# Performance work log

Hardware: AMD Instinct MI355X
Metric: run time of the kernel (lower is better)

## Reference

```python
import jax, jax.numpy as jnp
import numpy as np

NUM_USERS = 100000
NUM_ITEMS = 50000
DIM = 128
NUM_EDGES = 600000


def setup_inputs() -> dict:
    key = jax.random.key(0)
    k1, k2, k3, k4, k5, k6 = jax.random.split(key, 6)
    u_emb = jax.random.normal(k1, (NUM_USERS, DIM), dtype=jnp.float32)
    i_emb = jax.random.normal(k2, (NUM_ITEMS, DIM), dtype=jnp.float32)
    user_idx = jax.random.randint(k3, (NUM_EDGES,), 0, NUM_USERS, dtype=jnp.int32)
    item_idx = jax.random.randint(k4, (NUM_EDGES,), 0, NUM_ITEMS, dtype=jnp.int32)
    edge_index = jnp.stack([user_idx, item_idx], axis=0)
    # weights in [0.2, 1.0] per docstring (unused in eval-mode forward)
    weights = 0.2 + 0.8 * jax.random.uniform(k5, (NUM_EDGES,), dtype=jnp.float32)
    attn_w = jax.random.normal(k6, (2 * DIM,), dtype=jnp.float32) * (1.0 / np.sqrt(2 * DIM))
    return {"u_emb": u_emb, "i_emb": i_emb, "edge_index": edge_index,
            "weights": weights, "attn_w": attn_w}


def _scatter_softmax(scores, idx, num_nodes):
    # numerically stable segment softmax over edges grouped by idx
    smax = jax.ops.segment_max(scores, idx, num_segments=num_nodes)  # [N]
    exp_s = jnp.exp(scores - smax[idx])                              # [E]
    ssum = jax.ops.segment_sum(exp_s, idx, num_segments=num_nodes)   # [N]
    return exp_s / (ssum[idx] + 1e-10)


def reference(u_emb, i_emb, edge_index, weights, attn_w):
    num_users = u_emb.shape[0]
    num_items = i_emb.shape[0]
    dim = u_emb.shape[1]
    user_idx, item_idx = edge_index[0], edge_index[1]

    # attn_projector(cat([u, i])) == u @ w_u + i @ w_i (no bias)
    w_u, w_i = attn_w[:dim], attn_w[dim:]
    raw = u_emb[user_idx] @ w_u + i_emb[item_idx] @ w_i  # [E]
    raw = jnp.where(raw >= 0, raw, 0.2 * raw)            # LeakyReLU(0.2)

    u_attn = _scatter_softmax(raw, user_idx, num_users)  # [E]
    i_attn = _scatter_softmax(raw, item_idx, num_items)  # [E]

    new_u = u_emb.at[user_idx].add(i_emb[item_idx] * u_attn[:, None])
    new_i = i_emb.at[item_idx].add(u_emb[user_idx] * i_attn[:, None])
    return new_u, new_i
```

## Files before the change

kernel.cpp:

```cpp
#include <hip/hip_runtime.h>

#define DIM 128
#define SCAN_BLK 1024

__device__ __forceinline__ unsigned short bf16rn(float f) {
    unsigned u = __float_as_uint(f);
    u += 0x7fffu + ((u >> 16) & 1u);
    return (unsigned short)(u >> 16);
}

__global__ void k_prep(const float* __restrict__ u_emb, const float* __restrict__ i_emb,
                       const float* __restrict__ attn_w, float* __restrict__ sdot,
                       ushort2* __restrict__ bemb, unsigned* __restrict__ cnt,
                       int nu, int n, int do_bf16) {
    int tid = blockIdx.x * blockDim.x + threadIdx.x;
    if (tid < n) cnt[tid] = 0u;
    int gw = tid >> 6;
    int lane = threadIdx.x & 63;
    if (gw >= n) return;
    const bool isU = gw < nu;
    const float2* row = (const float2*)(isU ? u_emb + (size_t)gw * DIM
                                            : i_emb + (size_t)(gw - nu) * DIM);
    const float2* wv  = (const float2*)(isU ? attn_w : attn_w + DIM);
    float2 a = row[lane];
    float2 b = wv[lane];
    float v = a.x * b.x + a.y * b.y;
    #pragma unroll
    for (int off = 32; off; off >>= 1) v += __shfl_down(v, off);
    if (lane == 0) sdot[gw] = v;
    if (do_bf16) {
        ushort2 h;
        h.x = bf16rn(a.x);
        h.y = bf16rn(a.y);
        bemb[(size_t)gw * (DIM / 2) + lane] = h;
    }
}

__global__ void k_count(const int* __restrict__ uidx, const int* __restrict__ iidx,
                        unsigned* __restrict__ cnt, unsigned* __restrict__ ranks,
                        int nu, int ne) {
    int e = blockIdx.x * blockDim.x + threadIdx.x;
    if (e >= ne) return;
    unsigned r0 = atomicAdd(&cnt[uidx[e]], 1u);
    unsigned r1 = atomicAdd(&cnt[nu + iidx[e]], 1u);
    ranks[e] = (r0 << 16) | (r1 & 0xffffu);
}

__global__ void k_scan1(const unsigned* __restrict__ cnt, unsigned* __restrict__ incl,
                        unsigned* __restrict__ bsum, int n) {
    __shared__ unsigned part[SCAN_BLK];
    int t = threadIdx.x;
    int j = blockIdx.x * SCAN_BLK + t;
    unsigned v = (j < n) ? cnt[j] : 0u;
    part[t] = v;
    __syncthreads();
    for (int d = 1; d < SCAN_BLK; d <<= 1) {
        unsigned w = (t >= d) ? part[t - d] : 0u;
        __syncthreads();
        part[t] += w;
        __syncthreads();
    }
    if (j < n) incl[j] = part[t];
    if (t == SCAN_BLK - 1) bsum[blockIdx.x] = part[t];
}

__global__ void k_scan2(unsigned* __restrict__ bsum, int nb) {
    __shared__ unsigned part[SCAN_BLK];
    int t = threadIdx.x;
    unsigned v = (t < nb) ? bsum[t] : 0u;
    part[t] = v;
    __syncthreads();
    for (int d = 1; d < SCAN_BLK; d <<= 1) {
        unsigned w = (t >= d) ? part[t - d] : 0u;
        __syncthreads();
        part[t] += w;
        __syncthreads();
    }
    if (t < nb) bsum[t] = part[t] - v;
}

__global__ void k_scan3(const unsigned* __restrict__ cnt, const unsigned* __restrict__ incl,
                        const unsigned* __restrict__ bsum,
                        unsigned* __restrict__ off, int n) {
    int j = blockIdx.x * blockDim.x + threadIdx.x;
    if (j >= n) return;
    off[j] = incl[j] - cnt[j] + bsum[j / SCAN_BLK];
}

__global__ void k_fill(const int* __restrict__ uidx, const int* __restrict__ iidx,
                       const unsigned* __restrict__ off, const unsigned* __restrict__ ranks,
                       int* __restrict__ nbr, int nu, int ne) {
    int e = blockIdx.x * blockDim.x + threadIdx.x;
    if (e >= ne) return;
    int u = uidx[e], i = iidx[e];
    unsigned rk = ranks[e];
    nbr[off[u]      + (rk >> 16)]     = nu + i;
    nbr[off[nu + i] + (rk & 0xffffu)] = u;
}

__global__ void k_accum_bf16(const float* __restrict__ u_emb, const float* __restrict__ i_emb,
                             const uint4* __restrict__ bemb, const float* __restrict__ sdot,
                             const unsigned* __restrict__ off, const unsigned* __restrict__ cnt,
                             const int* __restrict__ nbr,
                             float* __restrict__ out, int nu, int n) {
    int gw   = (blockIdx.x * blockDim.x + threadIdx.x) >> 6;
    int lane = threadIdx.x & 63;
    int nwav = (gridDim.x * blockDim.x) >> 6;
    int q = lane >> 4, l16 = lane & 15;

    int node = gw;
    if (node >= n) return;

    unsigned sC = off[node], dC = cnt[node];
    float ssC = sdot[node];
    int oC = 0; float sdC = 0.f;
    {
        unsigned dc = dC < 64u ? dC : 64u;
        if ((unsigned)lane < dc) { oC = nbr[sC + lane]; sdC = sdot[oC]; }
    }

    while (true) {
        int nnode = node + nwav;
        unsigned sN = 0, dN = 0; float ssN = 0.f; int oN = 0; float sdN = 0.f;
        if (nnode < n) {
            sN = off[nnode]; dN = cnt[nnode]; ssN = sdot[nnode];
            unsigned dn = dN < 64u ? dN : 64u;
            if ((unsigned)lane < dn) { oN = nbr[sN + lane]; sdN = sdot[oN]; }
        }

        float acc[8] = {0.f, 0.f, 0.f, 0.f, 0.f, 0.f, 0.f, 0.f};
        float wsum = 0.f;

        auto doQuad = [&](int oArr, float wArr, int srcIdx, bool active) {
            int   oj = __shfl(oArr, srcIdx);
            float wj = __shfl(wArr, srcIdx);
            if (active) {
                uint4 h = bemb[(size_t)oj * (DIM / 8) + l16];
                wsum += wj;
                acc[0] += wj * __uint_as_float(h.x << 16);
                acc[1] += wj * __uint_as_float(h.x & 0xffff0000u);
                acc[2] += wj * __uint_as_float(h.y << 16);
                acc[3] += wj * __uint_as_float(h.y & 0xffff0000u);
                acc[4] += wj * __uint_as_float(h.z << 16);
                acc[5] += wj * __uint_as_float(h.z & 0xffff0000u);
                acc[6] += wj * __uint_as_float(h.w << 16);
                acc[7] += wj * __uint_as_float(h.w & 0xffff0000u);
            }
        };

        unsigned d0 = dC < 64u ? dC : 64u;
        float w = 0.f;
        if ((unsigned)lane < d0) {
            float r = ssC + sdC;
            r = fmaxf(r, 0.2f * r);
            w = __expf(r);
        }
        unsigned j = 0;
        #pragma unroll 4
        for (; j + 4 <= d0; j += 4) doQuad(oC, w, (int)j + q, true);
        if (j < d0)                 doQuad(oC, w, (int)(j + (unsigned)q), (unsigned)q < d0 - j);

        for (unsigned base = 64; base < dC; base += 64) {
            unsigned chunk = dC - base; if (chunk > 64) chunk = 64;
            int o2 = 0; float w2 = 0.f;
            if ((unsigned)lane < chunk) {
                o2 = nbr[sC + base + lane];
                float r = ssC + sdot[o2];
                r = fmaxf(r, 0.2f * r);
                w2 = __expf(r);
            }
            unsigned jj = 0;
            for (; jj + 4 <= chunk; jj += 4) doQuad(o2, w2, (int)jj + q, true);
            if (jj < chunk)                  doQuad(o2, w2, (int)(jj + (unsigned)q), (unsigned)q < chunk - jj);
        }

        #pragma unroll
        for (int m = 16; m <= 32; m <<= 1) {
            wsum += __shfl_xor(wsum, m);
            #pragma unroll
            for (int k = 0; k < 8; ++k) acc[k] += __shfl_xor(acc[k], m);
        }

        if (q == 0) {
            float inv = 1.f / (wsum + 1e-10f);
            const float* self = (node < nu) ? u_emb + (size_t)node * DIM
                                            : i_emb + (size_t)(node - nu) * DIM;
            const float4* sr = (const float4*)self;
            float4 s0 = sr[2 * l16];
            float4 s1 = sr[2 * l16 + 1];
            s0.x += acc[0] * inv; s0.y += acc[1] * inv;
            s0.z += acc[2] * inv; s0.w += acc[3] * inv;
            s1.x += acc[4] * inv; s1.y += acc[5] * inv;
            s1.z += acc[6] * inv; s1.w += acc[7] * inv;
            float4* orow = (float4*)(out + (size_t)node * DIM);
            orow[2 * l16]     = s0;
            orow[2 * l16 + 1] = s1;
        }

        if (nnode >= n) break;
        node = nnode;
        sC = sN; dC = dN; ssC = ssN; oC = oN; sdC = sdN;
    }
}

__global__ void k_accum_f32(const float* __restrict__ u_emb, const float* __restrict__ i_emb,
                            const float* __restrict__ sdot,
                            const unsigned* __restrict__ off, const unsigned* __restrict__ cnt,
                            const int* __restrict__ nbr,
                            float* __restrict__ out, int nu, int n) {
    int gw = (blockIdx.x * blockDim.x + threadIdx.x) >> 6;
    int lane = threadIdx.x & 63;
    if (gw >= n) return;
    float sd_self = sdot[gw];
    unsigned s = off[gw];
    unsigned d = cnt[gw];
    float2 acc = make_float2(0.f, 0.f);
    float wsum = 0.f;
    for (unsigned base = 0; base < d; base += 64) {
        unsigned chunk = d - base; if (chunk > 64) chunk = 64;
        int   o = 0;
        float w = 0.f;
        if (lane < (int)chunk) {
            o = nbr[s + base + lane];
            float r = sd_self + sdot[o];
            r = fmaxf(r, 0.2f * r);
            w = __expf(r);
        }
        for (unsigned j = 0; j < chunk; ++j) {
            int   oj = __shfl(o, (int)j);
            float wj = __shfl(w, (int)j);
            const float* base_ = (oj < nu) ? u_emb + (size_t)oj * DIM
                                           : i_emb + (size_t)(oj - nu) * DIM;
            float2 vj = ((const float2*)base_)[lane];
            wsum += wj;
            acc.x += wj * vj.x;
            acc.y += wj * vj.y;
        }
    }
    float inv = 1.f / (wsum + 1e-10f);
    const float* self = (gw < nu) ? u_emb + (size_t)gw * DIM
                                  : i_emb + (size_t)(gw - nu) * DIM;
    float2 sv = ((const float2*)self)[lane];
    sv.x += acc.x * inv;
    sv.y += acc.y * inv;
    ((float2*)(out + (size_t)gw * DIM))[lane] = sv;
}

extern "C" void kernel_launch(void* const* d_in, const int* in_sizes, int n_in,
                              void* d_out, int out_size, void* d_ws, size_t ws_size,
                              hipStream_t stream) {
    const float* u_emb  = (const float*)d_in[0];
    const float* i_emb  = (const float*)d_in[1];
    const int*   edge   = (const int*)d_in[2];
    const float* attn_w = (const float*)d_in[4];

    const int nu = in_sizes[0] / DIM;
    const int ni = in_sizes[1] / DIM;
    const int ne = in_sizes[3];
    const int n  = nu + ni;

    const int* uidx = edge;
    const int* iidx = edge + ne;

    float* out = (float*)d_out;

    char* ws = (char*)d_ws;
    size_t used = 0;
    auto take = [&](size_t bytes) {
        char* p = ws + used;
        used += (bytes + 15) & ~size_t(15);
        return p;
    };
    float*    sdot  = (float*)   take((size_t)n * sizeof(float));
    unsigned* cnt   = (unsigned*)take((size_t)n * sizeof(unsigned));
    unsigned* off   = (unsigned*)take((size_t)n * sizeof(unsigned));
    unsigned* incl  = (unsigned*)take((size_t)n * sizeof(unsigned));
    unsigned* bsum  = (unsigned*)take((size_t)SCAN_BLK * sizeof(unsigned));
    unsigned* ranks = (unsigned*)take((size_t)ne * sizeof(unsigned));
    int*      nbr   = (int*)     take((size_t)2 * ne * sizeof(int));
    size_t bembBytes = (size_t)n * DIM * 2;
    const int do_bf16 = (used + bembBytes <= ws_size) ? 1 : 0;
    void* bemb = do_bf16 ? (void*)take(bembBytes) : nullptr;

    const int nb = (n + SCAN_BLK - 1) / SCAN_BLK;

    k_prep<<<(n + 3) / 4, 256, 0, stream>>>(u_emb, i_emb, attn_w, sdot,
                                            (ushort2*)bemb, cnt, nu, n, do_bf16);

    k_count<<<(ne + 255) / 256, 256, 0, stream>>>(uidx, iidx, cnt, ranks, nu, ne);

    k_scan1<<<nb, SCAN_BLK, 0, stream>>>(cnt, incl, bsum, n);
    k_scan2<<<1, SCAN_BLK, 0, stream>>>(bsum, nb);
    k_scan3<<<(n + 255) / 256, 256, 0, stream>>>(cnt, incl, bsum, off, n);

    k_fill<<<(ne + 255) / 256, 256, 0, stream>>>(uidx, iidx, off, ranks, nbr, nu, ne);

    if (do_bf16)
        k_accum_bf16<<<2048, 256, 0, stream>>>(u_emb, i_emb, (const uint4*)bemb,
                                               sdot, off, cnt, nbr, out, nu, n);
    else
        k_accum_f32<<<(n + 3) / 4, 256, 0, stream>>>(u_emb, i_emb, sdot, off, cnt,
                                                     nbr, out, nu, n);
}
```

Before: 173.7 us.

## Process two nodes per wavefront iteration to interleave neighbor gathers

The bf16 accumulation kernel now handles two nodes (A and B) per wavefront loop iteration, interleaving their neighbor gathers in one loop over the larger degree, and prefetches the frontier data for the next pair. The goal is more independent memory loads in flight per wave to hide gather latency on the random bemb reads. The cost is roughly doubled accumulator registers, which may lower occupancy. Lanes also idle when the two degrees differ.

After: 204.2 us. 17.6% more time.

```diff
diff --git a/kernel.cpp b/kernel.cpp
--- a/kernel.cpp
+++ b/kernel.cpp
@@ -103,37 +103,55 @@
                              const unsigned* __restrict__ off, const unsigned* __restrict__ cnt,
                              const int* __restrict__ nbr,
                              float* __restrict__ out, int nu, int n) {
-    int gw   = (blockIdx.x * blockDim.x + threadIdx.x) >> 6;
+    int wid  = (blockIdx.x * blockDim.x + threadIdx.x) >> 6;
     int lane = threadIdx.x & 63;
     int nwav = (gridDim.x * blockDim.x) >> 6;
     int q = lane >> 4, l16 = lane & 15;
-
-    int node = gw;
-    if (node >= n) return;
-
-    unsigned sC = off[node], dC = cnt[node];
-    float ssC = sdot[node];
-    int oC = 0; float sdC = 0.f;
-    {
-        unsigned dc = dC < 64u ? dC : 64u;
-        if ((unsigned)lane < dc) { oC = nbr[sC + lane]; sdC = sdot[oC]; }
-    }
+    int step = 2 * nwav;
+
+    int nodeA = wid;
+    int nodeB = wid + nwav;
+    if (nodeA >= n) return;
+
+    auto loadFE = [&](int node, unsigned& s, unsigned& d, float& ss, int& o, float& sd) {
+        s = off[node]; d = cnt[node]; ss = sdot[node];
+        o = 0; sd = 0.f;
+        unsigned dc = d < 64u ? d : 64u;
+        if ((unsigned)lane < dc) { o = nbr[s + lane]; sd = sdot[o]; }
+    };
+
+    unsigned sA, dA, sB = 0, dB = 0;
+    float ssA, ssB = 0.f;
+    int oA, oB = 0;
+    float sdA, sdB = 0.f;
+    loadFE(nodeA, sA, dA, ssA, oA, sdA);
+    if (nodeB < n) loadFE(nodeB, sB, dB, ssB, oB, sdB);
 
     while (true) {
-        int nnode = node + nwav;
-        unsigned sN = 0, dN = 0; float ssN = 0.f; int oN = 0; float sdN = 0.f;
-        if (nnode < n) {
-            sN = off[nnode]; dN = cnt[nnode]; ssN = sdot[nnode];
-            unsigned dn = dN < 64u ? dN : 64u;
-            if ((unsigned)lane < dn) { oN = nbr[sN + lane]; sdN = sdot[oN]; }
-        }
-
-        float acc[8] = {0.f, 0.f, 0.f, 0.f, 0.f, 0.f, 0.f, 0.f};
-        float wsum = 0.f;
-
-        auto doQuad = [&](int oArr, float wArr, int srcIdx, bool active) {
-            int   oj = __shfl(oArr, srcIdx);
-            float wj = __shfl(wArr, srcIdx);
+        int nA = nodeA + step, nB = nodeB + step;
+        unsigned snA = 0, dnA = 0, snB = 0, dnB = 0;
+        float ssnA = 0.f, ssnB = 0.f, sdnA = 0.f, sdnB = 0.f;
+        int onA = 0, onB = 0;
+        if (nA < n) loadFE(nA, snA, dnA, ssnA, onA, sdnA);
+        if (nB < n) loadFE(nB, snB, dnB, ssnB, onB, sdnB);
+
+        float accA[8] = {0,0,0,0,0,0,0,0}, accB[8] = {0,0,0,0,0,0,0,0};
+        float wsumA = 0.f, wsumB = 0.f;
+
+        unsigned mA = dA < 64u ? dA : 64u;
+        unsigned mB = dB < 64u ? dB : 64u;
+        float wA = 0.f, wB = 0.f;
+        if ((unsigned)lane < mA) {
+            float r = ssA + sdA; r = fmaxf(r, 0.2f * r); wA = __expf(r);
+        }
+        if ((unsigned)lane < mB) {
+            float r = ssB + sdB; r = fmaxf(r, 0.2f * r); wB = __expf(r);
+        }
+
+        auto doQuad = [&](int oArr, float wArr, unsigned srcIdx, bool active,
+                          float* acc, float& wsum) {
+            int   oj = __shfl(oArr, (int)srcIdx);
+            float wj = __shfl(wArr, (int)srcIdx);
             if (active) {
                 uint4 h = bemb[(size_t)oj * (DIM / 8) + l16];
                 wsum += wj;
@@ -148,40 +166,51 @@
             }
         };
 
-        unsigned d0 = dC < 64u ? dC : 64u;
-        float w = 0.f;
-        if ((unsigned)lane < d0) {
-            float r = ssC + sdC;
-            r = fmaxf(r, 0.2f * r);
-            w = __expf(r);
-        }
-        unsigned j = 0;
-        #pragma unroll 4
-        for (; j + 4 <= d0; j += 4) doQuad(oC, w, (int)j + q, true);
-        if (j < d0)                 doQuad(oC, w, (int)(j + (unsigned)q), (unsigned)q < d0 - j);
-
-        for (unsigned base = 64; base < dC; base += 64) {
-            unsigned chunk = dC - base; if (chunk > 64) chunk = 64;
+        unsigned mx = mA > mB ? mA : mB;
+        #pragma unroll 2
+        for (unsigned j = 0; j < mx; j += 4) {
+            unsigned src = j + (unsigned)q;
+            doQuad(oA, wA, src, src < mA, accA, wsumA);
+            doQuad(oB, wB, src, src < mB, accB, wsumB);
+        }
+
+        for (unsigned base = 64; base < dA; base += 64) {
+            unsigned chunk = dA - base; if (chunk > 64) chunk = 64;
             int o2 = 0; float w2 = 0.f;
             if ((unsigned)lane < chunk) {
-                o2 = nbr[sC + base + lane];
-                float r = ssC + sdot[o2];
-                r = fmaxf(r, 0.2f * r);
-                w2 = __expf(r);
-            }
-            unsigned jj = 0;
-            for (; jj + 4 <= chunk; jj += 4) doQuad(o2, w2, (int)jj + q, true);
-            if (jj < chunk)                  doQuad(o2, w2, (int)(jj + (unsigned)q), (unsigned)q < chunk - jj);
+                o2 = nbr[sA + base + lane];
+                float r = ssA + sdot[o2]; r = fmaxf(r, 0.2f * r); w2 = __expf(r);
+            }
+            for (unsigned jj = 0; jj < chunk; jj += 4) {
+                unsigned src = jj + (unsigned)q;
+                doQuad(o2, w2, src, src < chunk, accA, wsumA);
+            }
+        }
+        for (unsigned base = 64; base < dB; base += 64) {
+            unsigned chunk = dB - base; if (chunk > 64) chunk = 64;
+            int o2 = 0; float w2 = 0.f;
+            if ((unsigned)lane < chunk) {
+                o2 = nbr[sB + base + lane];
+                float r = ssB + sdot[o2]; r = fmaxf(r, 0.2f * r); w2 = __expf(r);
+            }
+            for (unsigned jj = 0; jj < chunk; jj += 4) {
+                unsigned src = jj + (unsigned)q;
+                doQuad(o2, w2, src, src < chunk, accB, wsumB);
+            }
         }
 
         #pragma unroll
         for (int m = 16; m <= 32; m <<= 1) {
-            wsum += __shfl_xor(wsum, m);
+            wsumA += __shfl_xor(wsumA, m);
+            wsumB += __shfl_xor(wsumB, m);
             #pragma unroll
-            for (int k = 0; k < 8; ++k) acc[k] += __shfl_xor(acc[k], m);
-        }
-
-        if (q == 0) {
+            for (int k = 0; k < 8; ++k) {
+                accA[k] += __shfl_xor(accA[k], m);
+                accB[k] += __shfl_xor(accB[k], m);
+            }
+        }
+
+        auto writeRow = [&](int node, const float* acc, float wsum) {
             float inv = 1.f / (wsum + 1e-10f);
             const float* self = (node < nu) ? u_emb + (size_t)node * DIM
                                             : i_emb + (size_t)(node - nu) * DIM;
@@ -195,11 +224,16 @@
             float4* orow = (float4*)(out + (size_t)node * DIM);
             orow[2 * l16]     = s0;
             orow[2 * l16 + 1] = s1;
-        }
-
-        if (nnode >= n) break;
-        node = nnode;
-        sC = sN; dC = dN; ssC = ssN; oC = oN; sdC = sdN;
+        };
+        if (q == 0) {
+            writeRow(nodeA, accA, wsumA);
+            if (nodeB < n) writeRow(nodeB, accB, wsumB);
+        }
+
+        if (nA >= n) break;
+        nodeA = nA; nodeB = nB;
+        sA = snA; dA = dnA; ssA = ssnA; oA = onA; sdA = sdnA;
+        sB = snB; dB = dnB; ssB = ssnB; oB = onB; sdB = sdnB;
     }
 }
 
```
